# Kernel optimization log

Measured on AMD Instinct MI355X. Metric: run time of the kernel, lower is better.

## Reference

```python
import jax, jax.numpy as jnp
import numpy as np
import math

NHEAD = 8
NEG = -1e9  # stand-in for float('-inf') in the torch mask

def _layernorm(x, g, b):
    m = x.mean(-1, keepdims=True)
    v = ((x - m) ** 2).mean(-1, keepdims=True)
    return (x - m) / jnp.sqrt(v + 1e-5) * g + b

def setup_inputs() -> dict:
    key = jax.random.key(0)
    ks = jax.random.split(key, 8)
    B, S, D, E, F, L, C = 32, 512, 9, 256, 1024, 4, 10
    p = lambda k, shape: jax.random.normal(k, shape, dtype=jnp.float32) * 0.02
    return dict(
        src=jax.random.normal(ks[0], (B, S, D), dtype=jnp.float32),
        emb_W=p(ks[1], (E, D)), emb_b=jnp.zeros((E,), jnp.float32),
        Wqkv=p(ks[2], (L, 3 * E, E)), bqkv=jnp.zeros((L, 3 * E), jnp.float32),
        Wo=p(ks[3], (L, E, E)), bo=jnp.zeros((L, E), jnp.float32),
        ln1_g=jnp.ones((L, E), jnp.float32), ln1_b=jnp.zeros((L, E), jnp.float32),
        ln2_g=jnp.ones((L, E), jnp.float32), ln2_b=jnp.zeros((L, E), jnp.float32),
        W1=p(ks[4], (L, F, E)), b1=jnp.zeros((L, F), jnp.float32),
        W2=p(ks[5], (L, E, F)), b2=jnp.zeros((L, E), jnp.float32),
        dec_W=p(ks[6], (C, E)),
    )

def reference(src, emb_W, emb_b, Wqkv, bqkv, Wo, bo, ln1_g, ln1_b,
              ln2_g, ln2_b, W1, b1, W2, b2, dec_W):
    B, S, _ = src.shape
    E = emb_W.shape[0]
    H = NHEAD
    hd = E // H
    L = Wqkv.shape[0]

    # custom sparse mask: diagonal-only attention, except the last query row
    # attends to everything but itself (has_src_mask=True branch)
    eye = jnp.eye(S, dtype=src.dtype)
    mask = jnp.where(eye > 0, 0.0, NEG)
    mask = mask.at[-1, :].set(0.0).at[-1, -1].set(NEG)

    # sinusoidal positional encoding [S, E]
    pos = jnp.arange(S, dtype=jnp.float32)[:, None]
    div = jnp.exp(jnp.arange(0, E, 2, dtype=jnp.float32) * (-math.log(10000.0) / E))
    pe = jnp.zeros((S, E), jnp.float32)
    pe = pe.at[:, 0::2].set(jnp.sin(pos * div)).at[:, 1::2].set(jnp.cos(pos * div))

    # embed + scale + pos-enc (batch-first layout; math identical to seq-first)
    x = (src @ emb_W.T + emb_b) * math.sqrt(E) + pe[None, :, :]

    attns = []
    for l in range(L):  # small fixed number of layers
        qkv = x @ Wqkv[l].T + bqkv[l]  # [B,S,3E]
        q, k, v = jnp.split(qkv, 3, axis=-1)
        rs = lambda t: t.reshape(B, S, H, hd).transpose(0, 2, 1, 3)  # [B,H,S,hd]
        q, k, v = rs(q), rs(k), rs(v)
        scores = jnp.einsum('bhqd,bhkd->bhqk', q, k) / math.sqrt(hd) + mask
        a = jax.nn.softmax(scores, axis=-1)
        attns.append(a.mean(axis=1))  # head-averaged attention, as torch MHA returns
        o = jnp.einsum('bhqk,bhkd->bhqd', a, v).transpose(0, 2, 1, 3).reshape(B, S, E)
        x = _layernorm(x + (o @ Wo[l].T + bo[l]), ln1_g[l], ln1_b[l])
        f = jax.nn.relu(x @ W1[l].T + b1[l]) @ W2[l].T + b2[l]
        x = _layernorm(x + f, ln2_g[l], ln2_b[l])

    x = jax.nn.relu(x)
    out = (x @ dec_W.T).mean(axis=1)  # mean over sequence
    out = jax.nn.log_softmax(out, axis=-1)
    return out, jnp.stack(attns)
```

## Files before the change

kernel.cpp:

```cpp
#include <hip/hip_runtime.h>
#include <hip/hip_bf16.h>
#include <math.h>

namespace {

constexpr int BATCH = 32;
constexpr int SEQ   = 512;
constexpr int DIN   = 9;
constexpr int EMB   = 256;
constexpr int FF    = 1024;
constexpr int NLAYER= 4;
constexpr int NCLS  = 10;
constexpr int NHEADS= 8;
constexpr int HDIM  = 32;
constexpr int NTOK  = BATCH*SEQ;

typedef __attribute__((ext_vector_type(8))) short short8;
typedef __attribute__((ext_vector_type(4))) float floatx4;

#define GLOAD_LDS16(g, l) __builtin_amdgcn_global_load_lds( \
    (const __attribute__((address_space(1))) unsigned*)(g), \
    (__attribute__((address_space(3))) unsigned*)(l), 16, 0, 0)

#define WAITCNT(N) asm volatile("s_waitcnt vmcnt(" #N ")" ::: "memory")

template<bool RELU, bool KV>
__global__ __launch_bounds__(256)
void gemm_mfma(const __hip_bfloat16* __restrict__ A, int lda,
               const __hip_bfloat16* __restrict__ W,
               const float* __restrict__ bias,
               __hip_bfloat16* __restrict__ C0,
               __hip_bfloat16* __restrict__ C1,
               int ldc, int K)
{
    __shared__ __hip_bfloat16 As[2*128*32];
    __shared__ __hip_bfloat16 Bs[2*128*32];
    const int bm = blockIdx.y*128, bn = blockIdx.x*128;
    const int tid  = threadIdx.x;
    const int lane = tid & 63;
    const int w    = tid >> 6;
    const int wm   = (w >> 1)*64, wn = (w & 1)*64;

    floatx4 acc[4][4] = {};

    const int srow = w*32 + (lane >> 2);
    const int scol = (lane & 3)*8;
    const __hip_bfloat16* gA0 = A + (size_t)(bm + srow)*lda + scol;
    const __hip_bfloat16* gA1 = A + (size_t)(bm + srow + 16)*lda + scol;
    const __hip_bfloat16* gB0 = W + (size_t)(bn + srow)*K + scol;
    const __hip_bfloat16* gB1 = W + (size_t)(bn + srow + 16)*K + scol;
    const int l0 = (w*2)*512, l1 = (w*2 + 1)*512;

#define GM_STAGE(buf, k0) do { \
    GLOAD_LDS16(gA0 + (k0), As + (buf)*4096 + l0); \
    GLOAD_LDS16(gA1 + (k0), As + (buf)*4096 + l1); \
    GLOAD_LDS16(gB0 + (k0), Bs + (buf)*4096 + l0); \
    GLOAD_LDS16(gB1 + (k0), Bs + (buf)*4096 + l1); } while (0)

    const int arow = wm + (lane & 15);
    const int brow = wn + (lane & 15);
    const int kh   = lane >> 4;
    const int nt   = K >> 5;

    GM_STAGE(0, 0);
    for (int t = 0; t < nt; t++) {
        const int cur = t & 1;
        if (t + 1 < nt) {
            GM_STAGE(cur ^ 1, (t+1)*32);
            WAITCNT(4);
        } else {
            WAITCNT(0);
        }
        __builtin_amdgcn_s_barrier();
        const short8* Ab = (const short8*)(As + cur*4096);
        const short8* Bb = (const short8*)(Bs + cur*4096);
        short8 af[4], bf[4];
        #pragma unroll
        for (int m = 0; m < 4; m++) af[m] = Ab[(arow + m*16)*4 + kh];
        #pragma unroll
        for (int n = 0; n < 4; n++) bf[n] = Bb[(brow + n*16)*4 + kh];
        #pragma unroll
        for (int m = 0; m < 4; m++)
            #pragma unroll
            for (int n = 0; n < 4; n++)
                acc[m][n] = __builtin_amdgcn_mfma_f32_16x16x32_bf16(af[m], bf[n], acc[m][n], 0, 0, 0);
        __builtin_amdgcn_s_barrier();
    }
#undef GM_STAGE

    __hip_bfloat16* Cb;
    int cb;
    if (KV && bn >= 256) { Cb = C1; cb = bn - 256; }
    else                 { Cb = C0; cb = bn; }

    const int crow0 = bm + wm + (lane >> 4)*4;
    #pragma unroll
    for (int n = 0; n < 4; n++) {
        const int coln = wn + (lane & 15) + n*16;
        const float bv = bias[bn + coln];
        #pragma unroll
        for (int m = 0; m < 4; m++) {
            #pragma unroll
            for (int r = 0; r < 4; r++) {
                int row = crow0 + m*16 + r;
                float v = acc[m][n][r] + bv;
                if (RELU) v = fmaxf(v, 0.f);
                Cb[(size_t)row*ldc + cb + coln] = __float2bfloat16(v);
            }
        }
    }
}

__global__ __launch_bounds__(256)
void gemm_ln(const __hip_bfloat16* __restrict__ A, int lda,
             const __hip_bfloat16* __restrict__ W,
             const float* __restrict__ bias,
             const float* __restrict__ g,
             const float* __restrict__ bb,
             __hip_bfloat16* __restrict__ xb16,
             int K)
{
    __shared__ __hip_bfloat16 SM[2][18432];
    const int bm  = blockIdx.x*32;
    const int tid = threadIdx.x;
    const int lane= tid & 63;
    const int w   = tid >> 6;
    const int rgrp= w & 1;
    const int half= w >> 1;
    const int cl  = lane & 15;
    const int rg  = lane >> 4;
    const int Kh  = K >> 1;

    floatx4 acc[16] = {};

    const __hip_bfloat16* gsrc[9];
    int loff[9];
    #pragma unroll
    for (int i = 0; i < 9; i++) {
        int id = w*9 + i;
        if (id < 4) {
            int h = id >> 1, rc = id & 1;
            gsrc[i] = A + (size_t)(bm + rc*16 + (lane >> 2))*lda + h*Kh + (lane & 3)*8;
            loff[i] = h*1024 + rc*512;
        } else {
            int idb = id - 4;
            int h = idb >> 4, rc = idb & 15;
            gsrc[i] = W + (size_t)(rc*16 + (lane >> 2))*K + h*Kh + (lane & 3)*8;
            loff[i] = 2048 + h*8192 + rc*512;
        }
    }

#define GL2_STAGE(buf, k0) do { \
    _Pragma("unroll") \
    for (int i = 0; i < 9; i++) GLOAD_LDS16(gsrc[i] + (k0), &SM[buf][loff[i]]); } while (0)

    const int nt = Kh >> 5;
    GL2_STAGE(0, 0);
    const int aidx = half*128 + (rgrp*16 + cl)*4 + rg;
    for (int t = 0; t < nt; t++) {
        const int cur = t & 1;
        if (t + 1 < nt) {
            GL2_STAGE(cur ^ 1, (t+1)*32);
            WAITCNT(9);
        } else {
            WAITCNT(0);
        }
        __builtin_amdgcn_s_barrier();
        const short8* Sb = (const short8*)SM[cur];
        short8 af = Sb[aidx];
        #pragma unroll
        for (int n = 0; n < 16; n++) {
            short8 bf = Sb[256 + half*1024 + (n*16 + cl)*4 + rg];
            acc[n] = __builtin_amdgcn_mfma_f32_16x16x32_bf16(af, bf, acc[n], 0, 0, 0);
        }
        __builtin_amdgcn_s_barrier();
    }
#undef GL2_STAGE

    float* R = (float*)SM;
    if (half == 1) {
        #pragma unroll
        for (int n = 0; n < 16; n++)
            #pragma unroll
            for (int r = 0; r < 4; r++)
                R[rgrp*4096 + (n*4 + r)*64 + lane] = acc[n][r];
    }
    __syncthreads();
    if (half == 0) {
        #pragma unroll
        for (int n = 0; n < 16; n++)
            #pragma unroll
            for (int r = 0; r < 4; r++)
                acc[n][r] += R[rgrp*4096 + (n*4 + r)*64 + lane];

        float bv[16], gv[16], bbv[16];
        #pragma unroll
        for (int n = 0; n < 16; n++) {
            const int c = n*16 + cl;
            bv[n] = bias[c]; gv[n] = g[c]; bbv[n] = bb[c];
        }
        #pragma unroll
        for (int r = 0; r < 4; r++) {
            const int row = bm + rgrp*16 + rg*4 + r;
            __hip_bfloat16* xbr = xb16 + (size_t)row*EMB;
            float vals[16];
            float S = 0.f, Q = 0.f;
            #pragma unroll
            for (int n = 0; n < 16; n++) {
                float v = acc[n][r] + bv[n] + __bfloat162float(xbr[n*16 + cl]);
                vals[n] = v; S += v; Q += v*v;
            }
            #pragma unroll
            for (int o = 1; o < 16; o <<= 1) { S += __shfl_xor(S, o); Q += __shfl_xor(Q, o); }
            const float mean = S * (1.f/EMB);
            const float var  = Q * (1.f/EMB) - mean*mean;
            const float rstd = 1.f / sqrtf(var + 1e-5f);
            #pragma unroll
            for (int n = 0; n < 16; n++) {
                float v = (vals[n] - mean)*rstd*gv[n] + bbv[n];
                xbr[n*16 + cl] = __float2bfloat16(v);
            }
        }
    }
}

__global__ void f2b_all(const float* __restrict__ s0, const float* __restrict__ s1,
                        const float* __restrict__ s2, const float* __restrict__ s3,
                        __hip_bfloat16* __restrict__ d0, __hip_bfloat16* __restrict__ d1,
                        __hip_bfloat16* __restrict__ d2, __hip_bfloat16* __restrict__ d3)
{
    int blk = blockIdx.x;
    const float* s; __hip_bfloat16* d; int base;
    if      (blk <  768) { s = s0; d = d0; base = blk; }
    else if (blk < 1024) { s = s1; d = d1; base = blk - 768; }
    else if (blk < 2048) { s = s2; d = d2; base = blk - 1024; }
    else                 { s = s3; d = d3; base = blk - 2048; }
    int i = (base*256 + threadIdx.x)*4;
    float4 v = *(const float4*)(s + i);
    __hip_bfloat16 tmp[4];
    tmp[0] = __float2bfloat16(v.x); tmp[1] = __float2bfloat16(v.y);
    tmp[2] = __float2bfloat16(v.z); tmp[3] = __float2bfloat16(v.w);
    *(ushort4*)(d + i) = *(const ushort4*)tmp;
}

__global__ void embed_kernel(const float* __restrict__ src,
                             const float* __restrict__ emb_W,
                             const float* __restrict__ emb_b,
                             __hip_bfloat16* __restrict__ xb)
{
    int row = blockIdx.x;
    int e = threadIdx.x;
    int s = row % SEQ;
    const float* sr = src + (size_t)row*DIN;
    float acc = emb_b[e];
    #pragma unroll
    for (int d = 0; d < DIN; d++) acc += sr[d]*emb_W[e*DIN + d];
    acc *= 16.0f;
    int i2 = e & ~1;
    float div = expf(-(float)i2 * (9.210340371976184f / (float)EMB));
    float ang = (float)s * div;
    float pe = (e & 1) ? cosf(ang) : sinf(ang);
    xb[(size_t)row*EMB + e] = __float2bfloat16(acc + pe);
}

__global__ __launch_bounds__(512)
void attn_last_head(const __hip_bfloat16* __restrict__ xb,
                    const __hip_bfloat16* __restrict__ Wq,
                    const float* __restrict__ bq,
                    const __hip_bfloat16* __restrict__ kbuf,
                    __hip_bfloat16* __restrict__ vbuf,
                    float* __restrict__ amh)
{
    const int h = blockIdx.x, b = blockIdx.y;
    const int t = threadIdx.x;
    __shared__ float xlast[EMB];
    __shared__ float qpart[HDIM][17];
    __shared__ float qh[HDIM];
    __shared__ float sc[SEQ];
    __shared__ float red1[8], red2[8];
    __shared__ float opart[16][HDIM];

    if (t < EMB) xlast[t] = __bfloat162float(xb[((size_t)b*SEQ + SEQ-1)*EMB + t]);
    __syncthreads();

    {
        int d = t & 31, c = t >> 5;
        const __hip_bfloat16* wr = Wq + (size_t)(h*HDIM + d)*EMB + c*16;
        short8 w0 = *(const short8*)(wr);
        short8 w1 = *(const short8*)(wr + 8);
        float p = 0.f;
        #pragma unroll
        for (int j = 0; j < 8; j++)
            p += xlast[c*16 + j]*__bfloat162float(((const __hip_bfloat16*)&w0)[j]);
        #pragma unroll
        for (int j = 0; j < 8; j++)
            p += xlast[c*16 + 8 + j]*__bfloat162float(((const __hip_bfloat16*)&w1)[j]);
        qpart[d][c] = p;
    }
    __syncthreads();
    if (t < HDIM) {
        float qv = bq[h*HDIM + t];
        #pragma unroll
        for (int c = 0; c < 16; c++) qv += qpart[t][c];
        qh[t] = qv;
    }
    __syncthreads();

    {
        const __hip_bfloat16* krow = kbuf + ((size_t)b*SEQ + t)*EMB + h*HDIM;
        float s = 0.f;
        #pragma unroll
        for (int vv = 0; vv < 4; vv++) {
            short8 kk = *(const short8*)(krow + vv*8);
            #pragma unroll
            for (int j = 0; j < 8; j++)
                s += qh[vv*8 + j]*__bfloat162float(((const __hip_bfloat16*)&kk)[j]);
        }
        s *= 0.17677669529663687f;
        if (t == SEQ-1) s += -1e9f;
        sc[t] = s;
    }
    __syncthreads();

    {
        int wv = t >> 6, lane = t & 63;
        float m = sc[t];
        #pragma unroll
        for (int o = 32; o; o >>= 1) m = fmaxf(m, __shfl_xor(m, o));
        if (lane == 0) red1[wv] = m;
        __syncthreads();
        m = red1[0];
        #pragma unroll
        for (int i = 1; i < 8; i++) m = fmaxf(m, red1[i]);
        float e = expf(sc[t] - m);
        float s = e;
        #pragma unroll
        for (int o = 32; o; o >>= 1) s += __shfl_xor(s, o);
        if (lane == 0) red2[wv] = s;
        __syncthreads();
        float tot = red2[0]+red2[1]+red2[2]+red2[3]+red2[4]+red2[5]+red2[6]+red2[7];
        float a = e / tot;
        sc[t] = a;
        amh[((size_t)b*NHEADS + h)*SEQ + t] = a;
    }
    __syncthreads();

    {
        int e = t & 31, part = t >> 5;
        float o = 0.f;
        const __hip_bfloat16* vc = vbuf + (size_t)b*SEQ*EMB + h*HDIM + e;
        for (int k = part*32; k < part*32 + 32; k++)
            o += sc[k]*__bfloat162float(vc[(size_t)k*EMB]);
        opart[part][e] = o;
    }
    __syncthreads();
    if (t < HDIM) {
        float o = 0.f;
        #pragma unroll
        for (int p = 0; p < 16; p++) o += opart[p][t];
        vbuf[((size_t)b*SEQ + SEQ-1)*EMB + h*HDIM + t] = __float2bfloat16(o);
    }
}

__global__ void write_attns(float* __restrict__ attns, const float* __restrict__ amh_all)
{
    constexpr int PER_ROW = SEQ/4;
    size_t tid = (size_t)blockIdx.x*blockDim.x + threadIdx.x;
    size_t row = tid / PER_ROW;
    int c4 = (int)(tid % PER_ROW);
    int q = (int)(row % SEQ);
    float4 v = make_float4(0.f,0.f,0.f,0.f);
    if (q == SEQ-1) {
        size_t lb = row / SEQ;
        const float* base = amh_all + lb*NHEADS*SEQ + c4*4;
        float x0=0.f, x1=0.f, x2=0.f, x3=0.f;
        #pragma unroll
        for (int h = 0; h < NHEADS; h++) {
            const float* r = base + (size_t)h*SEQ;
            x0 += r[0]; x1 += r[1]; x2 += r[2]; x3 += r[3];
        }
        v = make_float4(x0*0.125f, x1*0.125f, x2*0.125f, x3*0.125f);
    } else if ((q >> 2) == c4) {
        ((float*)&v)[q & 3] = 1.f;
    }
    ((float4*)attns)[tid] = v;
}

__global__ __launch_bounds__(512)
void decode_fused(const __hip_bfloat16* __restrict__ xb, const float* __restrict__ dec_W,
                  float* __restrict__ out)
{
    int b = blockIdx.x, t = threadIdx.x;
    int e = t & 255, half = t >> 8;
    __shared__ float rs[2][256];
    {
        const __hip_bfloat16* xp = xb + ((size_t)b*SEQ + half*256)*EMB + e;
        float r = 0.f;
        for (int i = 0; i < 256; i++) r += fmaxf(__bfloat162float(xp[(size_t)i*EMB]), 0.f);
        rs[half][e] = r;
    }
    __syncthreads();
    float part[NCLS];
    if (t < 256) {
        float rr = rs[0][t] + rs[1][t];
        #pragma unroll
        for (int c = 0; c < NCLS; c++) part[c] = rr * dec_W[c*EMB + t];
    } else {
        #pragma unroll
        for (int c = 0; c < NCLS; c++) part[c] = 0.f;
    }
    #pragma unroll
    for (int o = 32; o; o >>= 1)
        #pragma unroll
        for (int c = 0; c < NCLS; c++) part[c] += __shfl_xor(part[c], o);
    __shared__ float red[8][NCLS];
    int wv = t >> 6, lane = t & 63;
    if (lane == 0)
        #pragma unroll
        for (int c = 0; c < NCLS; c++) red[wv][c] = part[c];
    __syncthreads();
    if (t == 0) {
        float lg[NCLS];
        float m = -1e30f;
        #pragma unroll
        for (int c = 0; c < NCLS; c++) {
            float s = 0.f;
            #pragma unroll
            for (int wvi = 0; wvi < 8; wvi++) s += red[wvi][c];
            lg[c] = s * (1.f/(float)SEQ);
            m = fmaxf(m, lg[c]);
        }
        float s = 0.f;
        #pragma unroll
        for (int c = 0; c < NCLS; c++) s += expf(lg[c] - m);
        float ls = logf(s);
        #pragma unroll
        for (int c = 0; c < NCLS; c++) out[b*NCLS + c] = lg[c] - m - ls;
    }
}

}

extern "C" void kernel_launch(void* const* d_in, const int* in_sizes, int n_in,
                              void* d_out, int out_size, void* d_ws, size_t ws_size,
                              hipStream_t stream)
{
    const float* src   = (const float*)d_in[0];
    const float* emb_W = (const float*)d_in[1];
    const float* emb_b = (const float*)d_in[2];
    const float* Wqkv  = (const float*)d_in[3];
    const float* bqkv  = (const float*)d_in[4];
    const float* Wo    = (const float*)d_in[5];
    const float* bo    = (const float*)d_in[6];
    const float* ln1_g = (const float*)d_in[7];
    const float* ln1_b = (const float*)d_in[8];
    const float* ln2_g = (const float*)d_in[9];
    const float* ln2_b = (const float*)d_in[10];
    const float* W1    = (const float*)d_in[11];
    const float* b1    = (const float*)d_in[12];
    const float* W2    = (const float*)d_in[13];
    const float* b2    = (const float*)d_in[14];
    const float* dec_W = (const float*)d_in[15];

    float* out   = (float*)d_out;
    float* attns = out + BATCH*NCLS;

    char* ws = (char*)d_ws;
    __hip_bfloat16* xb16 = (__hip_bfloat16*)ws;     ws += (size_t)NTOK*EMB*2;
    __hip_bfloat16* kbuf = (__hip_bfloat16*)ws;     ws += (size_t)NTOK*EMB*2;
    __hip_bfloat16* vbuf = (__hip_bfloat16*)ws;     ws += (size_t)NTOK*EMB*2;
    __hip_bfloat16* hbuf = (__hip_bfloat16*)ws;     ws += (size_t)NTOK*FF*2;
    __hip_bfloat16* wq16 = (__hip_bfloat16*)ws;     ws += (size_t)NLAYER*3*EMB*EMB*2;
    __hip_bfloat16* wo16 = (__hip_bfloat16*)ws;     ws += (size_t)NLAYER*EMB*EMB*2;
    __hip_bfloat16* w116 = (__hip_bfloat16*)ws;     ws += (size_t)NLAYER*FF*EMB*2;
    __hip_bfloat16* w216 = (__hip_bfloat16*)ws;     ws += (size_t)NLAYER*EMB*FF*2;
    float*          amall= (float*)ws;              ws += (size_t)NLAYER*BATCH*NHEADS*SEQ*4;

    f2b_all<<<3072, 256, 0, stream>>>(Wqkv, Wo, W1, W2, wq16, wo16, w116, w216);

    embed_kernel<<<NTOK, EMB, 0, stream>>>(src, emb_W, emb_b, xb16);

    for (int l = 0; l < NLAYER; l++) {
        const __hip_bfloat16* wql = wq16 + (size_t)l*3*EMB*EMB;
        const float* bql = bqkv + (size_t)l*3*EMB;

        gemm_mfma<false, true><<<dim3(512/128, NTOK/128), 256, 0, stream>>>(
            xb16, EMB, wql + (size_t)EMB*EMB, bql + EMB, kbuf, vbuf, EMB, EMB);

        attn_last_head<<<dim3(NHEADS, BATCH), 512, 0, stream>>>(
            xb16, wql, bql, kbuf, vbuf, amall + (size_t)l*BATCH*NHEADS*SEQ);

        gemm_ln<<<NTOK/32, 256, 0, stream>>>(
            vbuf, EMB, wo16 + (size_t)l*EMB*EMB, bo + (size_t)l*EMB,
            ln1_g + l*EMB, ln1_b + l*EMB, xb16, EMB);

        gemm_mfma<true, false><<<dim3(FF/128, NTOK/128), 256, 0, stream>>>(
            xb16, EMB, w116 + (size_t)l*FF*EMB, b1 + (size_t)l*FF, hbuf, nullptr, FF, EMB);

        gemm_ln<<<NTOK/32, 256, 0, stream>>>(
            hbuf, FF, w216 + (size_t)l*EMB*FF, b2 + (size_t)l*EMB,
            ln2_g + l*EMB, ln2_b + l*EMB, xb16, FF);
    }

    {
        size_t total_f4 = (size_t)NLAYER*BATCH*SEQ*(SEQ/4);
        int blocks = (int)((total_f4 + 255)/256);
        write_attns<<<blocks, 256, 0, stream>>>(attns, amall);
    }

    decode_fused<<<BATCH, 512, 0, stream>>>(xb16, dec_W, out);
}
```

Baseline: 546.7 us.

## Fuse out-projection, LN1, FFN and LN2 into one per-layer tail kernel

Replaces the Wo+LN1 GEMM, the W1 GEMM, and the W2+LN2 GEMM with a single layer_tail kernel per 32-row tile. The LN1 output and FFN hidden chunks stay in LDS, so the NTOK x FF hidden buffer is never written to or read from global memory. The last-row attention output goes to a small separate obuf, which the A-loader selects per row. Costs are more LDS and barriers per block, weights re-streamed per tile, and an M=32 tile that may underuse the MFMA units.

```diff
diff --git a/kernel.cpp b/kernel.cpp
--- a/kernel.cpp
+++ b/kernel.cpp
@@ -111,114 +111,204 @@
     }
 }
 
-__global__ __launch_bounds__(256)
-void gemm_ln(const __hip_bfloat16* __restrict__ A, int lda,
-             const __hip_bfloat16* __restrict__ W,
-             const float* __restrict__ bias,
-             const float* __restrict__ g,
-             const float* __restrict__ bb,
-             __hip_bfloat16* __restrict__ xb16,
-             int K)
-{
-    __shared__ __hip_bfloat16 SM[2][18432];
-    const int bm  = blockIdx.x*32;
-    const int tid = threadIdx.x;
-    const int lane= tid & 63;
-    const int w   = tid >> 6;
-    const int rgrp= w & 1;
-    const int half= w >> 1;
-    const int cl  = lane & 15;
-    const int rg  = lane >> 4;
-    const int Kh  = K >> 1;
-
-    floatx4 acc[16] = {};
-
-    const __hip_bfloat16* gsrc[9];
-    int loff[9];
+__device__ __forceinline__ void stageB(const __hip_bfloat16* __restrict__ W, int ldw,
+                                       int rowbase, int kbase,
+                                       __hip_bfloat16* LB, int buf, int w, int lane)
+{
     #pragma unroll
-    for (int i = 0; i < 9; i++) {
-        int id = w*9 + i;
-        if (id < 4) {
-            int h = id >> 1, rc = id & 1;
-            gsrc[i] = A + (size_t)(bm + rc*16 + (lane >> 2))*lda + h*Kh + (lane & 3)*8;
-            loff[i] = h*1024 + rc*512;
-        } else {
-            int idb = id - 4;
-            int h = idb >> 4, rc = idb & 15;
-            gsrc[i] = W + (size_t)(rc*16 + (lane >> 2))*K + h*Kh + (lane & 3)*8;
-            loff[i] = 2048 + h*8192 + rc*512;
-        }
-    }
-
-#define GL2_STAGE(buf, k0) do { \
-    _Pragma("unroll") \
-    for (int i = 0; i < 9; i++) GLOAD_LDS16(gsrc[i] + (k0), &SM[buf][loff[i]]); } while (0)
-
-    const int nt = Kh >> 5;
-    GL2_STAGE(0, 0);
-    const int aidx = half*128 + (rgrp*16 + cl)*4 + rg;
-    for (int t = 0; t < nt; t++) {
+    for (int i = 0; i < 4; i++) {
+        int rc = 4*w + i;
+        const __hip_bfloat16* src = W + (size_t)(rowbase + rc*16 + (lane >> 2))*ldw
+                                      + kbase + (lane & 3)*8;
+        GLOAD_LDS16(src, LB + buf*8192 + rc*512);
+    }
+}
+
+__device__ __forceinline__ void mfma8(const short8* Ab, const short8* Bb,
+                                      floatx4* acc, int rgrp, int colhalf,
+                                      int cl, int kh)
+{
+    short8 af = Ab[rgrp*64 + cl*4 + kh];
+    #pragma unroll
+    for (int n = 0; n < 8; n++) {
+        short8 bf = Bb[(colhalf*8 + n)*64 + cl*4 + kh];
+        acc[n] = __builtin_amdgcn_mfma_f32_16x16x32_bf16(af, bf, acc[n], 0, 0, 0);
+    }
+}
+
+__global__ __launch_bounds__(256, 2)
+void layer_tail(const __hip_bfloat16* __restrict__ vbuf,
+                const __hip_bfloat16* __restrict__ obuf,
+                const __hip_bfloat16* __restrict__ Wo,
+                const float* __restrict__ bo,
+                const float* __restrict__ g1, const float* __restrict__ b1ln,
+                const __hip_bfloat16* __restrict__ W1,
+                const float* __restrict__ b1f,
+                const __hip_bfloat16* __restrict__ W2,
+                const float* __restrict__ b2f,
+                const float* __restrict__ g2, const float* __restrict__ b2ln,
+                __hip_bfloat16* __restrict__ xb16)
+{
+    __shared__ __hip_bfloat16 SM[34816];
+    __hip_bfloat16* LB = SM;
+    __hip_bfloat16* LA = SM + 16384;
+    __hip_bfloat16* X1 = SM + 18432;
+    __hip_bfloat16* HC = SM + 26624;
+    float* RED = (float*)LA;
+
+    const int bm   = blockIdx.x*32;
+    const int tid  = threadIdx.x;
+    const int lane = tid & 63;
+    const int w    = tid >> 6;
+    const int rgrp = w & 1;
+    const int colhalf = w >> 1;
+    const int cl   = lane & 15;
+    const int rg   = lane >> 4;
+    const int kh   = lane >> 4;
+
+    floatx4 acc[8] = {};
+    const __hip_bfloat16* asrc = nullptr;
+    if (w >= 2) {
+        int a = w - 2;
+        int grow = bm + a*16 + (lane >> 2);
+        bool isl = (grow & (SEQ-1)) == (SEQ-1);
+        asrc = (isl ? obuf + (size_t)(grow >> 9)*EMB
+                    : vbuf + (size_t)grow*EMB) + (lane & 3)*8;
+    }
+    stageB(Wo, 256, 0, 0, LB, 0, w, lane);
+    if (w >= 2) GLOAD_LDS16(asrc, LA + (w-2)*512);
+    for (int t = 0; t < 8; t++) {
         const int cur = t & 1;
-        if (t + 1 < nt) {
-            GL2_STAGE(cur ^ 1, (t+1)*32);
-            WAITCNT(9);
-        } else {
-            WAITCNT(0);
-        }
+        if (t < 7) {
+            stageB(Wo, 256, 0, (t+1)*32, LB, cur^1, w, lane);
+            if (w >= 2) GLOAD_LDS16(asrc + (t+1)*32, LA + (cur^1)*1024 + (w-2)*512);
+            WAITCNT(4);
+        } else WAITCNT(0);
         __builtin_amdgcn_s_barrier();
-        const short8* Sb = (const short8*)SM[cur];
-        short8 af = Sb[aidx];
-        #pragma unroll
-        for (int n = 0; n < 16; n++) {
-            short8 bf = Sb[256 + half*1024 + (n*16 + cl)*4 + rg];
-            acc[n] = __builtin_amdgcn_mfma_f32_16x16x32_bf16(af, bf, acc[n], 0, 0, 0);
-        }
+        mfma8((const short8*)(LA + cur*1024), (const short8*)(LB + cur*8192),
+              acc, rgrp, colhalf, cl, kh);
         __builtin_amdgcn_s_barrier();
     }
-#undef GL2_STAGE
-
-    float* R = (float*)SM;
-    if (half == 1) {
-        #pragma unroll
-        for (int n = 0; n < 16; n++)
-            #pragma unroll
-            for (int r = 0; r < 4; r++)
-                R[rgrp*4096 + (n*4 + r)*64 + lane] = acc[n][r];
-    }
-    __syncthreads();
-    if (half == 0) {
-        #pragma unroll
-        for (int n = 0; n < 16; n++)
-            #pragma unroll
-            for (int r = 0; r < 4; r++)
-                acc[n][r] += R[rgrp*4096 + (n*4 + r)*64 + lane];
-
-        float bv[16], gv[16], bbv[16];
-        #pragma unroll
-        for (int n = 0; n < 16; n++) {
-            const int c = n*16 + cl;
-            bv[n] = bias[c]; gv[n] = g[c]; bbv[n] = bb[c];
+    {
+        float gv[8], bbv[8], bv[8];
+        #pragma unroll
+        for (int n = 0; n < 8; n++) {
+            int col = colhalf*128 + n*16 + cl;
+            bv[n] = bo[col]; gv[n] = g1[col]; bbv[n] = b1ln[col];
         }
         #pragma unroll
         for (int r = 0; r < 4; r++) {
-            const int row = bm + rgrp*16 + rg*4 + r;
-            __hip_bfloat16* xbr = xb16 + (size_t)row*EMB;
-            float vals[16];
+            int row = bm + rgrp*16 + rg*4 + r;
+            const __hip_bfloat16* xr = xb16 + (size_t)row*EMB + colhalf*128;
             float S = 0.f, Q = 0.f;
             #pragma unroll
-            for (int n = 0; n < 16; n++) {
-                float v = acc[n][r] + bv[n] + __bfloat162float(xbr[n*16 + cl]);
-                vals[n] = v; S += v; Q += v*v;
+            for (int n = 0; n < 8; n++) {
+                float v = acc[n][r] + bv[n] + __bfloat162float(xr[n*16 + cl]);
+                acc[n][r] = v; S += v; Q += v*v;
             }
             #pragma unroll
             for (int o = 1; o < 16; o <<= 1) { S += __shfl_xor(S, o); Q += __shfl_xor(Q, o); }
-            const float mean = S * (1.f/EMB);
-            const float var  = Q * (1.f/EMB) - mean*mean;
-            const float rstd = 1.f / sqrtf(var + 1e-5f);
-            #pragma unroll
-            for (int n = 0; n < 16; n++) {
-                float v = (vals[n] - mean)*rstd*gv[n] + bbv[n];
-                xbr[n*16 + cl] = __float2bfloat16(v);
+            if (cl == 0) {
+                int idx = rgrp*16 + rg*4 + r;
+                RED[colhalf*32 + idx] = S;
+                RED[64 + colhalf*32 + idx] = Q;
+            }
+        }
+        __syncthreads();
+        #pragma unroll
+        for (int r = 0; r < 4; r++) {
+            int idx = rgrp*16 + rg*4 + r;
+            float S = RED[idx] + RED[32 + idx];
+            float Q = RED[64 + idx] + RED[96 + idx];
+            float mean = S * (1.f/EMB);
+            float var  = Q * (1.f/EMB) - mean*mean;
+            float rstd = 1.f / sqrtf(var + 1e-5f);
+            #pragma unroll
+            for (int n = 0; n < 8; n++) {
+                int col = colhalf*128 + n*16 + cl;
+                float v = (acc[n][r] - mean)*rstd*gv[n] + bbv[n];
+                X1[(col >> 5)*1024 + rgrp*512 + (rg*4 + r)*32 + (col & 31)] = __float2bfloat16(v);
+            }
+        }
+        __syncthreads();
+    }
+
+    floatx4 acc2[8] = {};
+    for (int c = 0; c < 4; c++) {
+        floatx4 fa[8] = {};
+        stageB(W1, 256, c*256, 0, LB, 0, w, lane);
+        for (int t = 0; t < 8; t++) {
+            const int cur = t & 1;
+            if (t < 7) { stageB(W1, 256, c*256, (t+1)*32, LB, cur^1, w, lane); WAITCNT(4); }
+            else WAITCNT(0);
+            __builtin_amdgcn_s_barrier();
+            mfma8((const short8*)X1 + t*128, (const short8*)(LB + cur*8192),
+                  fa, rgrp, colhalf, cl, kh);
+            __builtin_amdgcn_s_barrier();
+        }
+        #pragma unroll
+        for (int n = 0; n < 8; n++) {
+            int colh = colhalf*128 + n*16 + cl;
+            float bb = b1f[c*256 + colh];
+            #pragma unroll
+            for (int r = 0; r < 4; r++) {
+                float v = fmaxf(fa[n][r] + bb, 0.f);
+                HC[(colh >> 5)*1024 + rgrp*512 + (rg*4 + r)*32 + (colh & 31)] = __float2bfloat16(v);
+            }
+        }
+        __syncthreads();
+        stageB(W2, 1024, 0, c*256, LB, 0, w, lane);
+        for (int t = 0; t < 8; t++) {
+            const int cur = t & 1;
+            if (t < 7) { stageB(W2, 1024, 0, c*256 + (t+1)*32, LB, cur^1, w, lane); WAITCNT(4); }
+            else WAITCNT(0);
+            __builtin_amdgcn_s_barrier();
+            mfma8((const short8*)HC + t*128, (const short8*)(LB + cur*8192),
+                  acc2, rgrp, colhalf, cl, kh);
+            __builtin_amdgcn_s_barrier();
+        }
+    }
+
+    {
+        float gv[8], bbv[8], bv[8];
+        #pragma unroll
+        for (int n = 0; n < 8; n++) {
+            int col = colhalf*128 + n*16 + cl;
+            bv[n] = b2f[col]; gv[n] = g2[col]; bbv[n] = b2ln[col];
+        }
+        #pragma unroll
+        for (int r = 0; r < 4; r++) {
+            float S = 0.f, Q = 0.f;
+            #pragma unroll
+            for (int n = 0; n < 8; n++) {
+                int col = colhalf*128 + n*16 + cl;
+                float x1v = __bfloat162float(X1[(col >> 5)*1024 + rgrp*512 + (rg*4 + r)*32 + (col & 31)]);
+                float v = acc2[n][r] + bv[n] + x1v;
+                acc2[n][r] = v; S += v; Q += v*v;
+            }
+            #pragma unroll
+            for (int o = 1; o < 16; o <<= 1) { S += __shfl_xor(S, o); Q += __shfl_xor(Q, o); }
+            if (cl == 0) {
+                int idx = rgrp*16 + rg*4 + r;
+                RED[colhalf*32 + idx] = S;
+                RED[64 + colhalf*32 + idx] = Q;
+            }
+        }
+        __syncthreads();
+        #pragma unroll
+        for (int r = 0; r < 4; r++) {
+            int idx = rgrp*16 + rg*4 + r;
+            int row = bm + idx;
+            float S = RED[idx] + RED[32 + idx];
+            float Q = RED[64 + idx] + RED[96 + idx];
+            float mean = S * (1.f/EMB);
+            float var  = Q * (1.f/EMB) - mean*mean;
+            float rstd = 1.f / sqrtf(var + 1e-5f);
+            __hip_bfloat16* xr = xb16 + (size_t)row*EMB + colhalf*128;
+            #pragma unroll
+            for (int n = 0; n < 8; n++) {
+                float v = (acc2[n][r] - mean)*rstd*gv[n] + bbv[n];
+                xr[n*16 + cl] = __float2bfloat16(v);
             }
         }
     }
@@ -268,7 +358,8 @@
                     const __hip_bfloat16* __restrict__ Wq,
                     const float* __restrict__ bq,
                     const __hip_bfloat16* __restrict__ kbuf,
-                    __hip_bfloat16* __restrict__ vbuf,
+                    const __hip_bfloat16* __restrict__ vbuf,
+                    __hip_bfloat16* __restrict__ obuf,
                     float* __restrict__ amh)
 {
     const int h = blockIdx.x, b = blockIdx.y;
@@ -358,7 +449,7 @@
         float o = 0.f;
         #pragma unroll
         for (int p = 0; p < 16; p++) o += opart[p][t];
-        vbuf[((size_t)b*SEQ + SEQ-1)*EMB + h*HDIM + t] = __float2bfloat16(o);
+        obuf[b*EMB + h*HDIM + t] = __float2bfloat16(o);
     }
 }
 
@@ -469,7 +560,7 @@
     __hip_bfloat16* xb16 = (__hip_bfloat16*)ws;     ws += (size_t)NTOK*EMB*2;
     __hip_bfloat16* kbuf = (__hip_bfloat16*)ws;     ws += (size_t)NTOK*EMB*2;
     __hip_bfloat16* vbuf = (__hip_bfloat16*)ws;     ws += (size_t)NTOK*EMB*2;
-    __hip_bfloat16* hbuf = (__hip_bfloat16*)ws;     ws += (size_t)NTOK*FF*2;
+    __hip_bfloat16* obuf = (__hip_bfloat16*)ws;     ws += (size_t)BATCH*EMB*2;
     __hip_bfloat16* wq16 = (__hip_bfloat16*)ws;     ws += (size_t)NLAYER*3*EMB*EMB*2;
     __hip_bfloat16* wo16 = (__hip_bfloat16*)ws;     ws += (size_t)NLAYER*EMB*EMB*2;
     __hip_bfloat16* w116 = (__hip_bfloat16*)ws;     ws += (size_t)NLAYER*FF*EMB*2;
@@ -488,18 +579,16 @@
             xb16, EMB, wql + (size_t)EMB*EMB, bql + EMB, kbuf, vbuf, EMB, EMB);
 
         attn_last_head<<<dim3(NHEADS, BATCH), 512, 0, stream>>>(
-            xb16, wql, bql, kbuf, vbuf, amall + (size_t)l*BATCH*NHEADS*SEQ);
-
-        gemm_ln<<<NTOK/32, 256, 0, stream>>>(
-            vbuf, EMB, wo16 + (size_t)l*EMB*EMB, bo + (size_t)l*EMB,
-            ln1_g + l*EMB, ln1_b + l*EMB, xb16, EMB);
-
-        gemm_mfma<true, false><<<dim3(FF/128, NTOK/128), 256, 0, stream>>>(
-            xb16, EMB, w116 + (size_t)l*FF*EMB, b1 + (size_t)l*FF, hbuf, nullptr, FF, EMB);
-
-        gemm_ln<<<NTOK/32, 256, 0, stream>>>(
-            hbuf, FF, w216 + (size_t)l*EMB*FF, b2 + (size_t)l*EMB,
-            ln2_g + l*EMB, ln2_b + l*EMB, xb16, FF);
+            xb16, wql, bql, kbuf, vbuf, obuf, amall + (size_t)l*BATCH*NHEADS*SEQ);
+
+        layer_tail<<<NTOK/32, 256, 0, stream>>>(
+            vbuf, obuf,
+            wo16 + (size_t)l*EMB*EMB, bo + (size_t)l*EMB,
+            ln1_g + l*EMB, ln1_b + l*EMB,
+            w116 + (size_t)l*FF*EMB, b1 + (size_t)l*FF,
+            w216 + (size_t)l*EMB*FF, b2 + (size_t)l*EMB,
+            ln2_g + l*EMB, ln2_b + l*EMB,
+            xb16);
     }
 
     {
```

Measured after the change: 486.2 us. -11.1%, faster.
